# Kernel tuning notes

Measured on AMD Instinct MI355X. Metric: run time of the kernel, lower is better.

Reference implementation:

```python
import jax, jax.numpy as jnp
import numpy as np
import math

H = 8
KAPPA = 20.0
STAGES = 10
BN_EPS = 1e-5


def _l2norm(x, axis):
    return x / (1e-6 + jnp.linalg.norm(x, axis=axis, keepdims=True))


def _pmms(node, query_feature, mu0):
    # node: (b,c,n)  query_feature: (b,n,c)  mu0: (1,c,k)
    b = node.shape[0]
    mu = jnp.broadcast_to(mu0, (b, mu0.shape[1], mu0.shape[2]))

    def step(mu, _):
        z = jax.nn.softmax(KAPPA * jnp.einsum('bcn,bck->bnk', node, mu), axis=2)
        z = z / (1e-6 + z.sum(axis=1, keepdims=True))
        mu = _l2norm(jnp.einsum('bcn,bnk->bck', node, z), axis=1)
        return mu, None

    mu, _ = jax.lax.scan(step, mu, None, length=STAGES)
    mu = jax.lax.stop_gradient(mu)  # torch.no_grad in EM
    P = jax.lax.stop_gradient(
        jax.nn.softmax(jnp.einsum('bnc,bck->bnk', query_feature, mu), axis=2))
    return P, mu


def _conv2d_same(x, w):
    return jax.lax.conv_general_dilated(
        x, w, (1, 1), 'SAME', dimension_numbers=('NCHW', 'OIHW', 'NCHW'))


def _node_weight(x, cw1, cb1, g, be, cw2, cb2):
    # x: (b, n, ch) with n a perfect square
    b, n, ch = x.shape
    w = int(math.isqrt(n))
    y = x.transpose(0, 2, 1).reshape(b * ch, 1, w, w)
    y = _conv2d_same(y, cw1) + cb1[None, :, None, None]
    # eval-mode BatchNorm2d (running_mean=0, running_var=1)
    y = g[None, :, None, None] * (y / jnp.sqrt(1.0 + BN_EPS)) + be[None, :, None, None]
    y = jax.nn.relu(y)
    y = _conv2d_same(y, cw2) + cb2[None, :, None, None]
    y = jax.nn.sigmoid(y)
    y = y.reshape(b, ch, n).transpose(0, 2, 1)
    return x * y


def setup_inputs() -> dict:
    key = jax.random.key(0)
    ks = jax.random.split(key, 16)
    b, n, d = 16, 1024, 256
    s = 0.02
    mu_a = _l2norm(jax.random.normal(ks[6], (1, d, 5), jnp.float32) * math.sqrt(2.0 / 5), axis=1)
    mu_b = _l2norm(jax.random.normal(ks[7], (1, d, 2), jnp.float32) * math.sqrt(2.0 / 2), axis=1)
    return {
        'query': jax.random.normal(ks[0], (b, n, d), jnp.float32),
        'key': jax.random.normal(ks[1], (b, n, d), jnp.float32),
        'value': jax.random.normal(ks[2], (b, n), jnp.float32),
        'lamda': jax.random.uniform(ks[3], (1,), jnp.float32),
        'W0': jax.random.normal(ks[4], (d, d), jnp.float32) * s,
        'b0': jnp.zeros((d,), jnp.float32),
        'W1': jax.random.normal(ks[5], (d, d), jnp.float32) * s,
        'b1': jnp.zeros((d,), jnp.float32),
        'mu_a': mu_a,
        'mu_b': mu_b,
        'nw1_w1': jax.random.normal(ks[8], (16, 1, 3, 3), jnp.float32) * 0.1,
        'nw1_b1': jnp.zeros((16,), jnp.float32),
        'nw1_g': jnp.ones((16,), jnp.float32),
        'nw1_be': jnp.zeros((16,), jnp.float32),
        'nw1_w2': jax.random.normal(ks[9], (1, 16, 3, 3), jnp.float32) * 0.1,
        'nw1_b2': jnp.zeros((1,), jnp.float32),
        'nw2_w1': jax.random.normal(ks[10], (16, 1, 3, 3), jnp.float32) * 0.1,
        'nw2_b1': jnp.zeros((16,), jnp.float32),
        'nw2_g': jnp.ones((16,), jnp.float32),
        'nw2_be': jnp.zeros((16,), jnp.float32),
        'nw2_w2': jax.random.normal(ks[11], (1, 16, 3, 3), jnp.float32) * 0.1,
        'nw2_b2': jnp.zeros((1,), jnp.float32),
    }


def reference(query, key, value, lamda, W0, b0, W1, b1, mu_a, mu_b,
              nw1_w1, nw1_b1, nw1_g, nw1_be, nw1_w2, nw1_b2,
              nw2_w1, nw2_b1, nw2_g, nw2_be, nw2_w2, nw2_b2):
    b, n, d = query.shape
    dk = d // H
    scale = 1.0 / math.sqrt(dk)
    # linear projections, split heads: (b,H,n,dk)
    q_l = (query @ W0.T + b0).reshape(b, n, H, dk).transpose(0, 2, 1, 3)
    k_l = (key @ W1.T + b1).reshape(b, n, H, dk).transpose(0, 2, 1, 3)
    v = value[:, None, :, None]  # (b,1,n,1) broadcast over heads
    # global path: value-weighted mean key, elementwise multiply-reduce, relu
    key_global = jnp.mean(k_l * v, axis=-2, keepdims=True)  # (b,H,1,dk)
    whole = jax.nn.relu(jnp.sum(q_l * key_global, axis=-1, keepdims=True) * scale)
    whole = jnp.mean(whole, axis=-3)  # (b,n,1)
    # local path: standard softmax attention with scalar values (dropout eval=identity)
    scores = jnp.einsum('bhqd,bhkd->bhqk', q_l, k_l) * scale
    p_attn = jax.nn.softmax(scores, axis=-1)
    part = jnp.einsum('bhqk,bk->bhq', p_attn, value)[..., None]  # (b,H,n,1)
    part = jnp.mean(part, axis=-3)  # (b,n,1)
    f = (1.0 - lamda) * part + lamda * whole
    # PMMs prototype clustering
    qT = query.transpose(0, 2, 1)  # (b,c,n)
    P1, m1 = _pmms(qT, query, mu_a)   # (b,n,5), (b,c,5)
    P2, _ = _pmms(m1, query, mu_b)    # (b,n,2)
    q1 = _node_weight(P1, nw1_w1, nw1_b1, nw1_g, nw1_be, nw1_w2, nw1_b2)
    q2 = _node_weight(P2, nw2_w1, nw2_b1, nw2_g, nw2_be, nw2_w2, nw2_b2)
    # tree_drop eval=identity
    return jnp.concatenate((f, q1, q2), axis=-1)  # (b,n,8)
```

## Files before the change

### kernel.cpp

```cpp
#include <hip/hip_runtime.h>
#include <hip/hip_bf16.h>
#include <math.h>

#define NN 1024
#define ND 256
#define PSTRIDE 1288

typedef __hip_bfloat16 bf;
__device__ __forceinline__ float bf2f(bf h) { return __bfloat162float(h); }

typedef __attribute__((ext_vector_type(8))) short bf16x8;
typedef __attribute__((ext_vector_type(4))) float f32x4;

__device__ __forceinline__ float wave_reduce_sum(float v) {
#pragma unroll
    for (int off = 32; off > 0; off >>= 1) v += __shfl_down(v, off, 64);
    return v;
}
__device__ __forceinline__ float wave_allreduce_sum(float v) {
#pragma unroll
    for (int off = 1; off < 64; off <<= 1) v += __shfl_xor(v, off, 64);
    return v;
}

__global__ void zero_k(float* __restrict__ out) {
    int i = blockIdx.x * 1024 + threadIdx.x;
    out[(size_t)i * 8] = 0.f;
}

__global__ __launch_bounds__(256) void gemm2_k(
    const float* __restrict__ Aq, const float* __restrict__ Ak,
    const float* __restrict__ W0, const float* __restrict__ b0v,
    const float* __restrict__ W1, const float* __restrict__ b1v,
    bf* __restrict__ QL, bf* __restrict__ KL)
{
    const float* A; const float* Bw; const float* bias; bf* C;
    if (blockIdx.z == 0) { A = Aq; Bw = W0; bias = b0v; C = QL; }
    else                 { A = Ak; Bw = W1; bias = b1v; C = KL; }
    __shared__ short Ahi[4 * 64 * 8],  Alo[4 * 64 * 8];
    __shared__ short Bhi[16 * 64 * 8], Blo[16 * 64 * 8];
    const int t = threadIdx.x;
    const int wave = t >> 6, lane = t & 63;
    const int m0 = blockIdx.x * 64;

    f32x4 acc[4][4];
#pragma unroll
    for (int m = 0; m < 4; m++)
#pragma unroll
        for (int n = 0; n < 4; n++)
#pragma unroll
            for (int r = 0; r < 4; r++) acc[m][n][r] = 0.f;

    for (int k0 = 0; k0 < 256; k0 += 32) {
        __syncthreads();
        {
            int fm = t >> 6, ls = t & 63;
            const float* src = A + (size_t)(m0 + fm * 16 + (ls & 15)) * 256 + k0 + ((ls >> 4) * 8);
            float4 x = *(const float4*)src;
            float4 y = *(const float4*)(src + 4);
            float v[8] = {x.x, x.y, x.z, x.w, y.x, y.y, y.z, y.w};
            short h[8], l8[8];
#pragma unroll
            for (int j = 0; j < 8; j++) {
                bf hb = __float2bfloat16(v[j]);
                float hf = __bfloat162float(hb);
                bf lb = __float2bfloat16(v[j] - hf);
                h[j] = *(short*)&hb; l8[j] = *(short*)&lb;
            }
            *(bf16x8*)&Ahi[t * 8] = *(bf16x8*)h;
            *(bf16x8*)&Alo[t * 8] = *(bf16x8*)l8;
        }
#pragma unroll
        for (int i = 0; i < 4; i++) {
            int idx = t + i * 256;
            int nf = idx >> 6, ls = idx & 63;
            const float* src = Bw + (size_t)(nf * 16 + (ls & 15)) * 256 + k0 + ((ls >> 4) * 8);
            float4 x = *(const float4*)src;
            float4 y = *(const float4*)(src + 4);
            float v[8] = {x.x, x.y, x.z, x.w, y.x, y.y, y.z, y.w};
            short h[8], l8[8];
#pragma unroll
            for (int j = 0; j < 8; j++) {
                bf hb = __float2bfloat16(v[j]);
                float hf = __bfloat162float(hb);
                bf lb = __float2bfloat16(v[j] - hf);
                h[j] = *(short*)&hb; l8[j] = *(short*)&lb;
            }
            *(bf16x8*)&Bhi[idx * 8] = *(bf16x8*)h;
            *(bf16x8*)&Blo[idx * 8] = *(bf16x8*)l8;
        }
        __syncthreads();
        bf16x8 ah[4], al[4], bh[4], bl[4];
#pragma unroll
        for (int m = 0; m < 4; m++) {
            ah[m] = *(const bf16x8*)&Ahi[(m * 64 + lane) * 8];
            al[m] = *(const bf16x8*)&Alo[(m * 64 + lane) * 8];
        }
#pragma unroll
        for (int n = 0; n < 4; n++) {
            int nf = wave * 4 + n;
            bh[n] = *(const bf16x8*)&Bhi[(nf * 64 + lane) * 8];
            bl[n] = *(const bf16x8*)&Blo[(nf * 64 + lane) * 8];
        }
#pragma unroll
        for (int m = 0; m < 4; m++)
#pragma unroll
            for (int n = 0; n < 4; n++) {
                acc[m][n] = __builtin_amdgcn_mfma_f32_16x16x32_bf16(ah[m], bh[n], acc[m][n], 0, 0, 0);
                acc[m][n] = __builtin_amdgcn_mfma_f32_16x16x32_bf16(ah[m], bl[n], acc[m][n], 0, 0, 0);
                acc[m][n] = __builtin_amdgcn_mfma_f32_16x16x32_bf16(al[m], bh[n], acc[m][n], 0, 0, 0);
            }
    }
#pragma unroll
    for (int n = 0; n < 4; n++) {
        int col = (wave * 4 + n) * 16 + (lane & 15);
        float bv = bias[col];
#pragma unroll
        for (int m = 0; m < 4; m++) {
            int row = m0 + m * 16 + (lane >> 4) * 4;
#pragma unroll
            for (int r = 0; r < 4; r++) {
                bf hv = __float2bfloat16(acc[m][n][r] + bv);
                C[(size_t)(row + r) * 256 + col] = hv;
            }
        }
    }
}

__global__ __launch_bounds__(256) void attn3_k(
    const bf* __restrict__ QL, const bf* __restrict__ KL,
    const float* __restrict__ value, const float* __restrict__ lamda,
    float* __restrict__ out)
{
    const int bh = blockIdx.x; const int b = bh >> 3, h = bh & 7;
    const int t = threadIdx.x;
    const int wave = t >> 6, lane = t & 63;
    const int q0 = blockIdx.y * 256 + wave * 64;
    const float scale = 0.17677669529663687f;

    __shared__ bf Kf[128 * 32];
    __shared__ float vv[128];

    bf16x8 qf[4];
    {
        const bf* qbase = QL + ((size_t)b * NN) * ND + h * 32 + (lane >> 4) * 8;
#pragma unroll
        for (int m = 0; m < 4; m++)
            qf[m] = *(const bf16x8*)(qbase + (size_t)(q0 + m * 16 + (lane & 15)) * ND);
    }
    f32x4 lsum[4], vacc[4], wacc[4];
#pragma unroll
    for (int m = 0; m < 4; m++)
#pragma unroll
        for (int r = 0; r < 4; r++) { lsum[m][r] = 0.f; vacc[m][r] = 0.f; wacc[m][r] = 0.f; }

    const bf* kbase = KL + ((size_t)b * NN) * ND + h * 32;
    for (int kt = 0; kt < 8; kt++) {
        const int k0 = kt * 128;
        __syncthreads();
#pragma unroll
        for (int i = 0; i < 2; i++) {
            int f = t + i * 256;
            int row = ((f >> 6) << 4) + (f & 15);
            int chunk = (f >> 4) & 3;
            *(bf16x8*)&Kf[f * 8] = *(const bf16x8*)(kbase + (size_t)(k0 + row) * ND + chunk * 8);
        }
        if (t < 128) vv[t] = value[(size_t)b * NN + k0 + t];
        __syncthreads();
#pragma unroll
        for (int s = 0; s < 8; s++) {
            bf16x8 bfr = *(const bf16x8*)&Kf[(s * 64 + lane) * 8];
            float vcol = vv[s * 16 + (lane & 15)];
#pragma unroll
            for (int m = 0; m < 4; m++) {
                f32x4 acc = {0.f, 0.f, 0.f, 0.f};
                acc = __builtin_amdgcn_mfma_f32_16x16x32_bf16(qf[m], bfr, acc, 0, 0, 0);
#pragma unroll
                for (int r = 0; r < 4; r++) {
                    float sraw = acc[r];
                    float p = __expf(sraw * scale);
                    lsum[m][r] += p;
                    vacc[m][r] += p * vcol;
                    wacc[m][r] += sraw * vcol;
                }
            }
        }
    }
    const float lam = lamda[0];
#pragma unroll
    for (int m = 0; m < 4; m++)
#pragma unroll
        for (int r = 0; r < 4; r++) {
            float ls = lsum[m][r], va = vacc[m][r], wa = wacc[m][r];
#pragma unroll
            for (int off = 1; off < 16; off <<= 1) {
                ls += __shfl_xor(ls, off, 64);
                va += __shfl_xor(va, off, 64);
                wa += __shfl_xor(wa, off, 64);
            }
            if ((lane & 15) == 0) {
                int q = q0 + m * 16 + (lane >> 4) * 4 + r;
                float part = va / ls;
                float whole = fmaxf(wa * scale * (1.0f / 1024.0f), 0.f);
                float f = ((1.f - lam) * part + lam * whole) * 0.125f;
                atomicAdd(&out[((size_t)b * NN + q) * 8], f);
            }
        }
}

__global__ __launch_bounds__(256) void pmms_a_k(
    const float* __restrict__ query, const float* __restrict__ mu0a,
    const float* __restrict__ pin, float* __restrict__ pout, int stage)
{
    __shared__ float qs[64 * 260];
    __shared__ float muT[5 * 256];
    __shared__ float z_s[64][8];
    __shared__ float red[32];
    int chunk = blockIdx.x, b = blockIdx.y;
    int t = threadIdx.x;
    int wave = t >> 6, lane = t & 63;

    {
        const float* qg = query + ((size_t)b * NN + chunk * 64) * ND;
        for (int i = t; i < 4096; i += 256) {
            int row = i >> 6, c4 = (i & 63) * 4;
            *(float4*)&qs[row * 260 + c4] = *(const float4*)&qg[(size_t)row * ND + c4];
        }
    }

    if (stage == 0) {
        for (int idx = t; idx < 1280; idx += 256)
            muT[idx] = mu0a[(idx & 255) * 5 + (idx >> 8)];
    } else {
        float mr[5] = {0,0,0,0,0};
        float cs[5] = {0,0,0,0,0};
        for (int ch = 0; ch < 16; ch++) {
            const float* pb = pin + ((size_t)(b * 16 + ch)) * PSTRIDE;
#pragma unroll
            for (int k = 0; k < 5; k++) mr[k] += pb[k * 256 + t];
#pragma unroll
            for (int k = 0; k < 5; k++) cs[k] += pb[1280 + k];
        }
#pragma unroll
        for (int k = 0; k < 5; k++) mr[k] *= 1.0f / (1e-6f + cs[k]);
#pragma unroll
        for (int k = 0; k < 5; k++) {
            float s = wave_reduce_sum(mr[k] * mr[k]);
            if (lane == 0) red[wave * 5 + k] = s;
        }
        __syncthreads();
        if (t < 5) red[20 + t] = 1.0f / (1e-6f + sqrtf(red[t] + red[5 + t] + red[10 + t] + red[15 + t]));
        __syncthreads();
#pragma unroll
        for (int k = 0; k < 5; k++) muT[k * 256 + t] = mr[k] * red[20 + k];
    }
    __syncthreads();

    int n_local = t >> 2, part = t & 3;
    const float* qrow = &qs[n_local * 260 + part * 64];
    float lg[5] = {0,0,0,0,0};
#pragma unroll
    for (int c4 = 0; c4 < 64; c4 += 4) {
        float4 qv = *(const float4*)&qrow[c4];
#pragma unroll
        for (int k = 0; k < 5; k++) {
            float4 mv = *(const float4*)&muT[k * 256 + part * 64 + c4];
            lg[k] += qv.x*mv.x + qv.y*mv.y + qv.z*mv.z + qv.w*mv.w;
        }
    }
#pragma unroll
    for (int k = 0; k < 5; k++) {
        lg[k] += __shfl_xor(lg[k], 1, 64);
        lg[k] += __shfl_xor(lg[k], 2, 64);
    }
    float mx = lg[0];
#pragma unroll
    for (int k = 1; k < 5; k++) mx = fmaxf(mx, lg[k]);
    float e[5], ssum = 0.f;
#pragma unroll
    for (int k = 0; k < 5; k++) { e[k] = expf(20.0f * (lg[k] - mx)); ssum += e[k]; }
    float is = 1.0f / ssum;
    if (part == 0) {
#pragma unroll
        for (int k = 0; k < 5; k++) z_s[n_local][k] = e[k] * is;
    }
    __syncthreads();

    float pa[5] = {0,0,0,0,0};
#pragma unroll 4
    for (int nl = 0; nl < 64; nl++) {
        float qv = qs[nl * 260 + t];
        float4 z4 = *(const float4*)&z_s[nl][0];
        float z4v = z_s[nl][4];
        pa[0] += qv * z4.x; pa[1] += qv * z4.y; pa[2] += qv * z4.z;
        pa[3] += qv * z4.w; pa[4] += qv * z4v;
    }
    float* pb = pout + ((size_t)(b * 16 + chunk)) * PSTRIDE;
#pragma unroll
    for (int k = 0; k < 5; k++) pb[k * 256 + t] = pa[k];
    if (t < 5) {
        float s = 0.f;
        for (int nl = 0; nl < 64; nl++) s += z_s[nl][t];
        pb[1280 + t] = s;
    }
}

__global__ __launch_bounds__(64) void pmms_b_k(
    const float* __restrict__ pin, const float* __restrict__ mu0b,
    float* __restrict__ m1_ws, float* __restrict__ mu2_ws)
{
    int b = blockIdx.x, lane = threadIdx.x;
    float nd[5][4];
    float cs[5] = {0,0,0,0,0};
#pragma unroll
    for (int n = 0; n < 5; n++)
#pragma unroll
        for (int j = 0; j < 4; j++) nd[n][j] = 0.f;
    for (int ch = 0; ch < 16; ch++) {
        const float* pb = pin + ((size_t)(b * 16 + ch)) * PSTRIDE;
#pragma unroll
        for (int n = 0; n < 5; n++)
#pragma unroll
            for (int j = 0; j < 4; j++) nd[n][j] += pb[n * 256 + lane + 64 * j];
#pragma unroll
        for (int n = 0; n < 5; n++) cs[n] += pb[1280 + n];
    }
#pragma unroll
    for (int n = 0; n < 5; n++) {
        float inv = 1.0f / (1e-6f + cs[n]);
        float sq = 0.f;
#pragma unroll
        for (int j = 0; j < 4; j++) { nd[n][j] *= inv; sq += nd[n][j] * nd[n][j]; }
        float s = wave_allreduce_sum(sq);
        float nr = 1.0f / (1e-6f + sqrtf(s));
#pragma unroll
        for (int j = 0; j < 4; j++) {
            nd[n][j] *= nr;
            m1_ws[((size_t)b * 5 + n) * 256 + lane + 64 * j] = nd[n][j];
        }
    }
    float mu[2][4];
#pragma unroll
    for (int k = 0; k < 2; k++)
#pragma unroll
        for (int j = 0; j < 4; j++) mu[k][j] = mu0b[(lane + 64 * j) * 2 + k];
    for (int stage = 0; stage < 10; stage++) {
        float z[5][2];
        float colsum0 = 0.f, colsum1 = 0.f;
#pragma unroll
        for (int n = 0; n < 5; n++) {
            float l0 = 0.f, l1 = 0.f;
#pragma unroll
            for (int j = 0; j < 4; j++) { l0 += nd[n][j] * mu[0][j]; l1 += nd[n][j] * mu[1][j]; }
            l0 = wave_allreduce_sum(l0);
            l1 = wave_allreduce_sum(l1);
            float a0 = 20.0f * l0, a1 = 20.0f * l1;
            float mxv = fmaxf(a0, a1);
            float e0 = expf(a0 - mxv), e1 = expf(a1 - mxv);
            float inv = 1.0f / (e0 + e1);
            z[n][0] = e0 * inv; z[n][1] = e1 * inv;
            colsum0 += z[n][0]; colsum1 += z[n][1];
        }
        float i0 = 1.0f / (1e-6f + colsum0), i1 = 1.0f / (1e-6f + colsum1);
#pragma unroll
        for (int k = 0; k < 2; k++) {
            float iv = k ? i1 : i0;
            float sq = 0.f;
            float nm[4];
#pragma unroll
            for (int j = 0; j < 4; j++) {
                float v = 0.f;
#pragma unroll
                for (int n = 0; n < 5; n++) v += nd[n][j] * z[n][k];
                v *= iv;
                nm[j] = v; sq += v * v;
            }
            float s = wave_allreduce_sum(sq);
            float nr = 1.0f / (1e-6f + sqrtf(s));
#pragma unroll
            for (int j = 0; j < 4; j++) mu[k][j] = nm[j] * nr;
        }
    }
#pragma unroll
    for (int k = 0; k < 2; k++)
#pragma unroll
        for (int j = 0; j < 4; j++) mu2_ws[((size_t)b * 2 + k) * 256 + lane + 64 * j] = mu[k][j];
}

__global__ __launch_bounds__(256) void pmap_k(
    const float* __restrict__ query, const float* __restrict__ m1_ws,
    const float* __restrict__ mu2_ws, float* __restrict__ P1, float* __restrict__ P2)
{
    __shared__ float ms[7 * 256];
    int b = blockIdx.y;
    int t = threadIdx.x;
    int n = blockIdx.x * 256 + t;
    for (int idx = t; idx < 1280; idx += 256) ms[idx] = m1_ws[(size_t)b * 1280 + idx];
    for (int idx = t; idx < 512; idx += 256) ms[1280 + idx] = mu2_ws[(size_t)b * 512 + idx];
    __syncthreads();
    const float* qrow = query + ((size_t)b * NN + n) * ND;
    float lg[7] = {0,0,0,0,0,0,0};
    for (int c4 = 0; c4 < 256; c4 += 4) {
        float4 qv = *(const float4*)&qrow[c4];
#pragma unroll
        for (int k = 0; k < 7; k++) {
            float4 mv = *(const float4*)&ms[k * 256 + c4];
            lg[k] += qv.x*mv.x + qv.y*mv.y + qv.z*mv.z + qv.w*mv.w;
        }
    }
    float mx = lg[0];
#pragma unroll
    for (int k = 1; k < 5; k++) mx = fmaxf(mx, lg[k]);
    float e[5], ssum = 0.f;
#pragma unroll
    for (int k = 0; k < 5; k++) { e[k] = expf(lg[k] - mx); ssum += e[k]; }
    float is = 1.0f / ssum;
#pragma unroll
    for (int k = 0; k < 5; k++) P1[((size_t)b * 5 + k) * NN + n] = e[k] * is;
    float mx2 = fmaxf(lg[5], lg[6]);
    float e0 = expf(lg[5] - mx2), e1 = expf(lg[6] - mx2);
    float inv = 1.0f / (e0 + e1);
    P2[((size_t)b * 2 + 0) * NN + n] = e0 * inv;
    P2[((size_t)b * 2 + 1) * NN + n] = e1 * inv;
}

__global__ __launch_bounds__(1024) void nwconv_k(
    const float* __restrict__ P1, const float* __restrict__ P2,
    const float* __restrict__ w1a, const float* __restrict__ b1a,
    const float* __restrict__ ga,  const float* __restrict__ bea,
    const float* __restrict__ w2a, const float* __restrict__ b2a,
    const float* __restrict__ w1b, const float* __restrict__ b1b,
    const float* __restrict__ gb,  const float* __restrict__ beb,
    const float* __restrict__ w2b, const float* __restrict__ b2b,
    float* __restrict__ out)
{
    __shared__ float img[34 * 34];
    __shared__ float mid[16][34 * 34];
    __shared__ float w1s[144], w2s[144], bs[16], gs[16], bes[16], b2s[1];
    int ch = blockIdx.x, b = blockIdx.y;
    int t = threadIdx.x;
    int i = t >> 5, j = t & 31;
    const float* xsrc = (ch < 5) ? &P1[((size_t)b * 5 + ch) * NN]
                                 : &P2[((size_t)b * 2 + (ch - 5)) * NN];
    if (t < 144) { w1s[t] = (ch < 5 ? w1a : w1b)[t]; w2s[t] = (ch < 5 ? w2a : w2b)[t]; }
    if (t >= 256 && t < 272) {
        int y = t - 256;
        bs[y] = (ch < 5 ? b1a : b1b)[y];
        gs[y] = (ch < 5 ? ga : gb)[y];
        bes[y] = (ch < 5 ? bea : beb)[y];
    }
    if (t == 512) b2s[0] = (ch < 5 ? b2a : b2b)[0];
    for (int idx = t; idx < 1156; idx += 1024) img[idx] = 0.f;
    for (int idx = t; idx < 16 * 1156; idx += 1024) ((float*)mid)[idx] = 0.f;
    __syncthreads();
    float xv = xsrc[t];
    img[(i + 1) * 34 + (j + 1)] = xv;
    __syncthreads();
    float r[9];
#pragma unroll
    for (int dy = 0; dy < 3; dy++)
#pragma unroll
        for (int dx = 0; dx < 3; dx++)
            r[dy * 3 + dx] = img[(i + dy) * 34 + (j + dx)];
    const float bninv = rsqrtf(1.0f + 1e-5f);
#pragma unroll
    for (int oc = 0; oc < 16; oc++) {
        float a = 0.f;
#pragma unroll
        for (int q2 = 0; q2 < 9; q2++) a += w1s[oc * 9 + q2] * r[q2];
        a += bs[oc];
        a = gs[oc] * (a * bninv) + bes[oc];
        a = fmaxf(a, 0.f);
        mid[oc][(i + 1) * 34 + (j + 1)] = a;
    }
    __syncthreads();
    float acc2 = b2s[0];
#pragma unroll
    for (int oc = 0; oc < 16; oc++)
#pragma unroll
        for (int dy = 0; dy < 3; dy++)
#pragma unroll
            for (int dx = 0; dx < 3; dx++)
                acc2 += w2s[oc * 9 + dy * 3 + dx] * mid[oc][(i + dy) * 34 + (j + dx)];
    float sig = 1.0f / (1.0f + expf(-acc2));
    out[((size_t)(b * NN + t)) * 8 + 1 + ch] = xv * sig;
}

extern "C" void kernel_launch(void* const* d_in, const int* in_sizes, int n_in,
                              void* d_out, int out_size, void* d_ws, size_t ws_size,
                              hipStream_t stream) {
    const float* query = (const float*)d_in[0];
    const float* key   = (const float*)d_in[1];
    const float* value = (const float*)d_in[2];
    const float* lamda = (const float*)d_in[3];
    const float* W0 = (const float*)d_in[4];
    const float* b0 = (const float*)d_in[5];
    const float* W1 = (const float*)d_in[6];
    const float* b1 = (const float*)d_in[7];
    const float* mu_a = (const float*)d_in[8];
    const float* mu_b = (const float*)d_in[9];
    const float* nw1_w1 = (const float*)d_in[10];
    const float* nw1_b1 = (const float*)d_in[11];
    const float* nw1_g  = (const float*)d_in[12];
    const float* nw1_be = (const float*)d_in[13];
    const float* nw1_w2 = (const float*)d_in[14];
    const float* nw1_b2 = (const float*)d_in[15];
    const float* nw2_w1 = (const float*)d_in[16];
    const float* nw2_b1 = (const float*)d_in[17];
    const float* nw2_g  = (const float*)d_in[18];
    const float* nw2_be = (const float*)d_in[19];
    const float* nw2_w2 = (const float*)d_in[20];
    const float* nw2_b2 = (const float*)d_in[21];
    float* out = (float*)d_out;

    bf* QLb = (bf*)d_ws;
    bf* KLb = (bf*)((char*)d_ws + ((size_t)8 << 20));
    float* PA   = (float*)d_ws;
    float* PB   = PA + (size_t)16 * 16 * PSTRIDE;
    float* m1w  = PB + (size_t)16 * 16 * PSTRIDE;
    float* mu2w = m1w + (size_t)16 * 1280;
    float* P1w  = mu2w + (size_t)16 * 512;
    float* P2w  = P1w + (size_t)16 * 5 * 1024;

    zero_k<<<16, 1024, 0, stream>>>(out);
    gemm2_k<<<dim3(256, 1, 2), 256, 0, stream>>>(query, key, W0, b0, W1, b1, QLb, KLb);
    attn3_k<<<dim3(128, 4), 256, 0, stream>>>(QLb, KLb, value, lamda, out);
    for (int s = 0; s < 10; s++) {
        const float* pin = (s & 1) ? PA : PB;
        float* pout      = (s & 1) ? PB : PA;
        pmms_a_k<<<dim3(16, 16), 256, 0, stream>>>(query, mu_a, pin, pout, s);
    }
    pmms_b_k<<<16, 64, 0, stream>>>(PB, mu_b, m1w, mu2w);
    pmap_k<<<dim3(4, 16), 256, 0, stream>>>(query, m1w, mu2w, P1w, P2w);
    nwconv_k<<<dim3(7, 16), 1024, 0, stream>>>(P1w, P2w,
                                    nw1_w1, nw1_b1, nw1_g, nw1_be, nw1_w2, nw1_b2,
                                    nw2_w1, nw2_b1, nw2_g, nw2_be, nw2_w2, nw2_b2, out);
}
```

Baseline: 397.1 us.

## Fuse PMMs stages into one cooperative kernel and fold attention scale into QL

Replaces the ten per-stage PMMs launches, the second-level EM kernel and the probability-map kernel with a single cooperative kernel that keeps the query tile in LDS and uses grid-wide syncs between stages. This removes repeated launch overhead and the query reload on every stage. Separately, the attention scale times log2(e) is folded into the QL projection so attention can use exp2 directly, and the attention grid is doubled with half the rows per wave for more parallelism. Risks include grid-sync cost, co-residency requirements for the cooperative launch, and slight precision changes from bf16-rounding the scaled Q.

```diff
diff --git a/kernel.cpp b/kernel.cpp
--- a/kernel.cpp
+++ b/kernel.cpp
@@ -1,16 +1,21 @@
 #include <hip/hip_runtime.h>
 #include <hip/hip_bf16.h>
+#include <hip/hip_cooperative_groups.h>
 #include <math.h>
+
+namespace cg = cooperative_groups;
 
 #define NN 1024
 #define ND 256
 #define PSTRIDE 1288
 
 typedef __hip_bfloat16 bf;
-__device__ __forceinline__ float bf2f(bf h) { return __bfloat162float(h); }
 
 typedef __attribute__((ext_vector_type(8))) short bf16x8;
 typedef __attribute__((ext_vector_type(4))) float f32x4;
+
+#define QL_ALPHA 0.25503486216f
+#define WHOLE_LN2 0.6931471805599453f
 
 __device__ __forceinline__ float wave_reduce_sum(float v) {
 #pragma unroll
@@ -34,9 +39,9 @@
     const float* __restrict__ W1, const float* __restrict__ b1v,
     bf* __restrict__ QL, bf* __restrict__ KL)
 {
-    const float* A; const float* Bw; const float* bias; bf* C;
-    if (blockIdx.z == 0) { A = Aq; Bw = W0; bias = b0v; C = QL; }
-    else                 { A = Ak; Bw = W1; bias = b1v; C = KL; }
+    const float* A; const float* Bw; const float* bias; bf* C; float alpha;
+    if (blockIdx.z == 0) { A = Aq; Bw = W0; bias = b0v; C = QL; alpha = QL_ALPHA; }
+    else                 { A = Ak; Bw = W1; bias = b1v; C = KL; alpha = 1.0f; }
     __shared__ short Ahi[4 * 64 * 8],  Alo[4 * 64 * 8];
     __shared__ short Bhi[16 * 64 * 8], Blo[16 * 64 * 8];
     const int t = threadIdx.x;
@@ -120,14 +125,14 @@
             int row = m0 + m * 16 + (lane >> 4) * 4;
 #pragma unroll
             for (int r = 0; r < 4; r++) {
-                bf hv = __float2bfloat16(acc[m][n][r] + bv);
+                bf hv = __float2bfloat16((acc[m][n][r] + bv) * alpha);
                 C[(size_t)(row + r) * 256 + col] = hv;
             }
         }
     }
 }
 
-__global__ __launch_bounds__(256) void attn3_k(
+__global__ __launch_bounds__(256) void attn4_k(
     const bf* __restrict__ QL, const bf* __restrict__ KL,
     const float* __restrict__ value, const float* __restrict__ lamda,
     float* __restrict__ out)
@@ -135,22 +140,21 @@
     const int bh = blockIdx.x; const int b = bh >> 3, h = bh & 7;
     const int t = threadIdx.x;
     const int wave = t >> 6, lane = t & 63;
-    const int q0 = blockIdx.y * 256 + wave * 64;
-    const float scale = 0.17677669529663687f;
+    const int q0 = blockIdx.y * 128 + wave * 32;
 
     __shared__ bf Kf[128 * 32];
     __shared__ float vv[128];
 
-    bf16x8 qf[4];
+    bf16x8 qf[2];
     {
         const bf* qbase = QL + ((size_t)b * NN) * ND + h * 32 + (lane >> 4) * 8;
 #pragma unroll
-        for (int m = 0; m < 4; m++)
+        for (int m = 0; m < 2; m++)
             qf[m] = *(const bf16x8*)(qbase + (size_t)(q0 + m * 16 + (lane & 15)) * ND);
     }
-    f32x4 lsum[4], vacc[4], wacc[4];
-#pragma unroll
-    for (int m = 0; m < 4; m++)
+    f32x4 lsum[2], vacc[2], wacc[2];
+#pragma unroll
+    for (int m = 0; m < 2; m++)
 #pragma unroll
         for (int r = 0; r < 4; r++) { lsum[m][r] = 0.f; vacc[m][r] = 0.f; wacc[m][r] = 0.f; }
 
@@ -172,13 +176,13 @@
             bf16x8 bfr = *(const bf16x8*)&Kf[(s * 64 + lane) * 8];
             float vcol = vv[s * 16 + (lane & 15)];
 #pragma unroll
-            for (int m = 0; m < 4; m++) {
+            for (int m = 0; m < 2; m++) {
                 f32x4 acc = {0.f, 0.f, 0.f, 0.f};
                 acc = __builtin_amdgcn_mfma_f32_16x16x32_bf16(qf[m], bfr, acc, 0, 0, 0);
 #pragma unroll
                 for (int r = 0; r < 4; r++) {
                     float sraw = acc[r];
-                    float p = __expf(sraw * scale);
+                    float p = exp2f(sraw);
                     lsum[m][r] += p;
                     vacc[m][r] += p * vcol;
                     wacc[m][r] += sraw * vcol;
@@ -188,7 +192,7 @@
     }
     const float lam = lamda[0];
 #pragma unroll
-    for (int m = 0; m < 4; m++)
+    for (int m = 0; m < 2; m++)
 #pragma unroll
         for (int r = 0; r < 4; r++) {
             float ls = lsum[m][r], va = vacc[m][r], wa = wacc[m][r];
@@ -201,24 +205,30 @@
             if ((lane & 15) == 0) {
                 int q = q0 + m * 16 + (lane >> 4) * 4 + r;
                 float part = va / ls;
-                float whole = fmaxf(wa * scale * (1.0f / 1024.0f), 0.f);
+                float whole = fmaxf(wa * (WHOLE_LN2 / 1024.0f), 0.f);
                 float f = ((1.f - lam) * part + lam * whole) * 0.125f;
                 atomicAdd(&out[((size_t)b * NN + q) * 8], f);
             }
         }
 }
 
-__global__ __launch_bounds__(256) void pmms_a_k(
+__global__ __launch_bounds__(256) void pmms_coop_k(
     const float* __restrict__ query, const float* __restrict__ mu0a,
-    const float* __restrict__ pin, float* __restrict__ pout, int stage)
+    const float* __restrict__ mu0b,
+    float* __restrict__ PA, float* __restrict__ PB,
+    float* __restrict__ m1w, float* __restrict__ mu2w,
+    float* __restrict__ P1, float* __restrict__ P2)
 {
+    cg::grid_group gg = cg::this_grid();
     __shared__ float qs[64 * 260];
     __shared__ float muT[5 * 256];
+    __shared__ float ms2[512];
     __shared__ float z_s[64][8];
     __shared__ float red[32];
-    int chunk = blockIdx.x, b = blockIdx.y;
-    int t = threadIdx.x;
-    int wave = t >> 6, lane = t & 63;
+    const int chunk = blockIdx.x, b = blockIdx.y;
+    const int t = threadIdx.x;
+    const int wave = t >> 6, lane = t & 63;
+    const int n_local = t >> 2, part = t & 3;
 
     {
         const float* qg = query + ((size_t)b * NN + chunk * 64) * ND;
@@ -228,200 +238,215 @@
         }
     }
 
-    if (stage == 0) {
-        for (int idx = t; idx < 1280; idx += 256)
-            muT[idx] = mu0a[(idx & 255) * 5 + (idx >> 8)];
-    } else {
-        float mr[5] = {0,0,0,0,0};
+    for (int stage = 0; stage < 10; stage++) {
+        const float* pin = (stage & 1) ? PA : PB;
+        float* pout      = (stage & 1) ? PB : PA;
+        if (stage == 0) {
+            for (int idx = t; idx < 1280; idx += 256)
+                muT[idx] = mu0a[(idx & 255) * 5 + (idx >> 8)];
+        } else {
+            float mr[5] = {0,0,0,0,0};
+            float cs[5] = {0,0,0,0,0};
+            for (int ch = 0; ch < 16; ch++) {
+                const float* pb = pin + ((size_t)(b * 16 + ch)) * PSTRIDE;
+#pragma unroll
+                for (int k = 0; k < 5; k++) mr[k] += pb[k * 256 + t];
+#pragma unroll
+                for (int k = 0; k < 5; k++) cs[k] += pb[1280 + k];
+            }
+#pragma unroll
+            for (int k = 0; k < 5; k++) mr[k] *= 1.0f / (1e-6f + cs[k]);
+#pragma unroll
+            for (int k = 0; k < 5; k++) {
+                float s = wave_reduce_sum(mr[k] * mr[k]);
+                if (lane == 0) red[wave * 5 + k] = s;
+            }
+            __syncthreads();
+            if (t < 5) red[20 + t] = 1.0f / (1e-6f + sqrtf(red[t] + red[5 + t] + red[10 + t] + red[15 + t]));
+            __syncthreads();
+#pragma unroll
+            for (int k = 0; k < 5; k++) muT[k * 256 + t] = mr[k] * red[20 + k];
+        }
+        __syncthreads();
+
+        {
+            const float* qrow = &qs[n_local * 260 + part * 64];
+            float lg[5] = {0,0,0,0,0};
+#pragma unroll
+            for (int c4 = 0; c4 < 64; c4 += 4) {
+                float4 qv = *(const float4*)&qrow[c4];
+#pragma unroll
+                for (int k = 0; k < 5; k++) {
+                    float4 mv = *(const float4*)&muT[k * 256 + part * 64 + c4];
+                    lg[k] += qv.x*mv.x + qv.y*mv.y + qv.z*mv.z + qv.w*mv.w;
+                }
+            }
+#pragma unroll
+            for (int k = 0; k < 5; k++) {
+                lg[k] += __shfl_xor(lg[k], 1, 64);
+                lg[k] += __shfl_xor(lg[k], 2, 64);
+            }
+            float mx = lg[0];
+#pragma unroll
+            for (int k = 1; k < 5; k++) mx = fmaxf(mx, lg[k]);
+            float e[5], ssum = 0.f;
+#pragma unroll
+            for (int k = 0; k < 5; k++) { e[k] = expf(20.0f * (lg[k] - mx)); ssum += e[k]; }
+            float is = 1.0f / ssum;
+            if (part == 0) {
+#pragma unroll
+                for (int k = 0; k < 5; k++) z_s[n_local][k] = e[k] * is;
+            }
+        }
+        __syncthreads();
+
+        {
+            float pa[5] = {0,0,0,0,0};
+#pragma unroll 4
+            for (int nl = 0; nl < 64; nl++) {
+                float qv = qs[nl * 260 + t];
+                float4 z4 = *(const float4*)&z_s[nl][0];
+                float z4v = z_s[nl][4];
+                pa[0] += qv * z4.x; pa[1] += qv * z4.y; pa[2] += qv * z4.z;
+                pa[3] += qv * z4.w; pa[4] += qv * z4v;
+            }
+            float* pb = pout + ((size_t)(b * 16 + chunk)) * PSTRIDE;
+#pragma unroll
+            for (int k = 0; k < 5; k++) pb[k * 256 + t] = pa[k];
+            if (t < 5) {
+                float s = 0.f;
+                for (int nl = 0; nl < 64; nl++) s += z_s[nl][t];
+                pb[1280 + t] = s;
+            }
+        }
+        __threadfence();
+        gg.sync();
+    }
+
+    if (chunk == 0 && t < 64) {
+        const int ln = t;
+        float nd[5][4];
         float cs[5] = {0,0,0,0,0};
+#pragma unroll
+        for (int n = 0; n < 5; n++)
+#pragma unroll
+            for (int j = 0; j < 4; j++) nd[n][j] = 0.f;
         for (int ch = 0; ch < 16; ch++) {
-            const float* pb = pin + ((size_t)(b * 16 + ch)) * PSTRIDE;
-#pragma unroll
-            for (int k = 0; k < 5; k++) mr[k] += pb[k * 256 + t];
-#pragma unroll
-            for (int k = 0; k < 5; k++) cs[k] += pb[1280 + k];
-        }
-#pragma unroll
-        for (int k = 0; k < 5; k++) mr[k] *= 1.0f / (1e-6f + cs[k]);
-#pragma unroll
-        for (int k = 0; k < 5; k++) {
-            float s = wave_reduce_sum(mr[k] * mr[k]);
-            if (lane == 0) red[wave * 5 + k] = s;
-        }
-        __syncthreads();
-        if (t < 5) red[20 + t] = 1.0f / (1e-6f + sqrtf(red[t] + red[5 + t] + red[10 + t] + red[15 + t]));
-        __syncthreads();
-#pragma unroll
-        for (int k = 0; k < 5; k++) muT[k * 256 + t] = mr[k] * red[20 + k];
-    }
-    __syncthreads();
-
-    int n_local = t >> 2, part = t & 3;
-    const float* qrow = &qs[n_local * 260 + part * 64];
-    float lg[5] = {0,0,0,0,0};
-#pragma unroll
-    for (int c4 = 0; c4 < 64; c4 += 4) {
-        float4 qv = *(const float4*)&qrow[c4];
-#pragma unroll
-        for (int k = 0; k < 5; k++) {
-            float4 mv = *(const float4*)&muT[k * 256 + part * 64 + c4];
-            lg[k] += qv.x*mv.x + qv.y*mv.y + qv.z*mv.z + qv.w*mv.w;
-        }
-    }
-#pragma unroll
-    for (int k = 0; k < 5; k++) {
-        lg[k] += __shfl_xor(lg[k], 1, 64);
-        lg[k] += __shfl_xor(lg[k], 2, 64);
-    }
-    float mx = lg[0];
-#pragma unroll
-    for (int k = 1; k < 5; k++) mx = fmaxf(mx, lg[k]);
-    float e[5], ssum = 0.f;
-#pragma unroll
-    for (int k = 0; k < 5; k++) { e[k] = expf(20.0f * (lg[k] - mx)); ssum += e[k]; }
-    float is = 1.0f / ssum;
-    if (part == 0) {
-#pragma unroll
-        for (int k = 0; k < 5; k++) z_s[n_local][k] = e[k] * is;
-    }
-    __syncthreads();
-
-    float pa[5] = {0,0,0,0,0};
-#pragma unroll 4
-    for (int nl = 0; nl < 64; nl++) {
-        float qv = qs[nl * 260 + t];
-        float4 z4 = *(const float4*)&z_s[nl][0];
-        float z4v = z_s[nl][4];
-        pa[0] += qv * z4.x; pa[1] += qv * z4.y; pa[2] += qv * z4.z;
-        pa[3] += qv * z4.w; pa[4] += qv * z4v;
-    }
-    float* pb = pout + ((size_t)(b * 16 + chunk)) * PSTRIDE;
-#pragma unroll
-    for (int k = 0; k < 5; k++) pb[k * 256 + t] = pa[k];
-    if (t < 5) {
-        float s = 0.f;
-        for (int nl = 0; nl < 64; nl++) s += z_s[nl][t];
-        pb[1280 + t] = s;
-    }
-}
-
-__global__ __launch_bounds__(64) void pmms_b_k(
-    const float* __restrict__ pin, const float* __restrict__ mu0b,
-    float* __restrict__ m1_ws, float* __restrict__ mu2_ws)
-{
-    int b = blockIdx.x, lane = threadIdx.x;
-    float nd[5][4];
-    float cs[5] = {0,0,0,0,0};
-#pragma unroll
-    for (int n = 0; n < 5; n++)
-#pragma unroll
-        for (int j = 0; j < 4; j++) nd[n][j] = 0.f;
-    for (int ch = 0; ch < 16; ch++) {
-        const float* pb = pin + ((size_t)(b * 16 + ch)) * PSTRIDE;
-#pragma unroll
-        for (int n = 0; n < 5; n++)
-#pragma unroll
-            for (int j = 0; j < 4; j++) nd[n][j] += pb[n * 256 + lane + 64 * j];
-#pragma unroll
-        for (int n = 0; n < 5; n++) cs[n] += pb[1280 + n];
-    }
-#pragma unroll
-    for (int n = 0; n < 5; n++) {
-        float inv = 1.0f / (1e-6f + cs[n]);
-        float sq = 0.f;
-#pragma unroll
-        for (int j = 0; j < 4; j++) { nd[n][j] *= inv; sq += nd[n][j] * nd[n][j]; }
-        float s = wave_allreduce_sum(sq);
-        float nr = 1.0f / (1e-6f + sqrtf(s));
-#pragma unroll
-        for (int j = 0; j < 4; j++) {
-            nd[n][j] *= nr;
-            m1_ws[((size_t)b * 5 + n) * 256 + lane + 64 * j] = nd[n][j];
-        }
-    }
-    float mu[2][4];
-#pragma unroll
-    for (int k = 0; k < 2; k++)
-#pragma unroll
-        for (int j = 0; j < 4; j++) mu[k][j] = mu0b[(lane + 64 * j) * 2 + k];
-    for (int stage = 0; stage < 10; stage++) {
-        float z[5][2];
-        float colsum0 = 0.f, colsum1 = 0.f;
+            const float* pb = PB + ((size_t)(b * 16 + ch)) * PSTRIDE;
+#pragma unroll
+            for (int n = 0; n < 5; n++)
+#pragma unroll
+                for (int j = 0; j < 4; j++) nd[n][j] += pb[n * 256 + ln + 64 * j];
+#pragma unroll
+            for (int n = 0; n < 5; n++) cs[n] += pb[1280 + n];
+        }
 #pragma unroll
         for (int n = 0; n < 5; n++) {
-            float l0 = 0.f, l1 = 0.f;
-#pragma unroll
-            for (int j = 0; j < 4; j++) { l0 += nd[n][j] * mu[0][j]; l1 += nd[n][j] * mu[1][j]; }
-            l0 = wave_allreduce_sum(l0);
-            l1 = wave_allreduce_sum(l1);
-            float a0 = 20.0f * l0, a1 = 20.0f * l1;
-            float mxv = fmaxf(a0, a1);
-            float e0 = expf(a0 - mxv), e1 = expf(a1 - mxv);
-            float inv = 1.0f / (e0 + e1);
-            z[n][0] = e0 * inv; z[n][1] = e1 * inv;
-            colsum0 += z[n][0]; colsum1 += z[n][1];
-        }
-        float i0 = 1.0f / (1e-6f + colsum0), i1 = 1.0f / (1e-6f + colsum1);
-#pragma unroll
-        for (int k = 0; k < 2; k++) {
-            float iv = k ? i1 : i0;
+            float inv = 1.0f / (1e-6f + cs[n]);
             float sq = 0.f;
-            float nm[4];
-#pragma unroll
-            for (int j = 0; j < 4; j++) {
-                float v = 0.f;
-#pragma unroll
-                for (int n = 0; n < 5; n++) v += nd[n][j] * z[n][k];
-                v *= iv;
-                nm[j] = v; sq += v * v;
-            }
+#pragma unroll
+            for (int j = 0; j < 4; j++) { nd[n][j] *= inv; sq += nd[n][j] * nd[n][j]; }
             float s = wave_allreduce_sum(sq);
             float nr = 1.0f / (1e-6f + sqrtf(s));
 #pragma unroll
-            for (int j = 0; j < 4; j++) mu[k][j] = nm[j] * nr;
-        }
-    }
-#pragma unroll
-    for (int k = 0; k < 2; k++)
-#pragma unroll
-        for (int j = 0; j < 4; j++) mu2_ws[((size_t)b * 2 + k) * 256 + lane + 64 * j] = mu[k][j];
-}
-
-__global__ __launch_bounds__(256) void pmap_k(
-    const float* __restrict__ query, const float* __restrict__ m1_ws,
-    const float* __restrict__ mu2_ws, float* __restrict__ P1, float* __restrict__ P2)
-{
-    __shared__ float ms[7 * 256];
-    int b = blockIdx.y;
-    int t = threadIdx.x;
-    int n = blockIdx.x * 256 + t;
-    for (int idx = t; idx < 1280; idx += 256) ms[idx] = m1_ws[(size_t)b * 1280 + idx];
-    for (int idx = t; idx < 512; idx += 256) ms[1280 + idx] = mu2_ws[(size_t)b * 512 + idx];
+            for (int j = 0; j < 4; j++) {
+                nd[n][j] *= nr;
+                m1w[((size_t)b * 5 + n) * 256 + ln + 64 * j] = nd[n][j];
+            }
+        }
+        float mu[2][4];
+#pragma unroll
+        for (int k = 0; k < 2; k++)
+#pragma unroll
+            for (int j = 0; j < 4; j++) mu[k][j] = mu0b[(ln + 64 * j) * 2 + k];
+        for (int stage = 0; stage < 10; stage++) {
+            float z[5][2];
+            float colsum0 = 0.f, colsum1 = 0.f;
+#pragma unroll
+            for (int n = 0; n < 5; n++) {
+                float l0 = 0.f, l1 = 0.f;
+#pragma unroll
+                for (int j = 0; j < 4; j++) { l0 += nd[n][j] * mu[0][j]; l1 += nd[n][j] * mu[1][j]; }
+                l0 = wave_allreduce_sum(l0);
+                l1 = wave_allreduce_sum(l1);
+                float a0 = 20.0f * l0, a1 = 20.0f * l1;
+                float mxv = fmaxf(a0, a1);
+                float e0 = expf(a0 - mxv), e1 = expf(a1 - mxv);
+                float inv = 1.0f / (e0 + e1);
+                z[n][0] = e0 * inv; z[n][1] = e1 * inv;
+                colsum0 += z[n][0]; colsum1 += z[n][1];
+            }
+            float i0 = 1.0f / (1e-6f + colsum0), i1 = 1.0f / (1e-6f + colsum1);
+#pragma unroll
+            for (int k = 0; k < 2; k++) {
+                float iv = k ? i1 : i0;
+                float sq = 0.f;
+                float nm[4];
+#pragma unroll
+                for (int j = 0; j < 4; j++) {
+                    float v = 0.f;
+#pragma unroll
+                    for (int n = 0; n < 5; n++) v += nd[n][j] * z[n][k];
+                    v *= iv;
+                    nm[j] = v; sq += v * v;
+                }
+                float s = wave_allreduce_sum(sq);
+                float nr = 1.0f / (1e-6f + sqrtf(s));
+#pragma unroll
+                for (int j = 0; j < 4; j++) mu[k][j] = nm[j] * nr;
+            }
+        }
+#pragma unroll
+        for (int k = 0; k < 2; k++)
+#pragma unroll
+            for (int j = 0; j < 4; j++) mu2w[((size_t)b * 2 + k) * 256 + ln + 64 * j] = mu[k][j];
+    }
+    __threadfence();
+    gg.sync();
+
+    for (int idx = t; idx < 1280; idx += 256) muT[idx] = m1w[(size_t)b * 1280 + idx];
+    for (int idx = t; idx < 512; idx += 256) ms2[idx] = mu2w[(size_t)b * 512 + idx];
     __syncthreads();
-    const float* qrow = query + ((size_t)b * NN + n) * ND;
-    float lg[7] = {0,0,0,0,0,0,0};
-    for (int c4 = 0; c4 < 256; c4 += 4) {
-        float4 qv = *(const float4*)&qrow[c4];
+    {
+        const float* qrow = &qs[n_local * 260 + part * 64];
+        float lg[7] = {0,0,0,0,0,0,0};
+#pragma unroll
+        for (int c4 = 0; c4 < 64; c4 += 4) {
+            float4 qv = *(const float4*)&qrow[c4];
+#pragma unroll
+            for (int k = 0; k < 5; k++) {
+                float4 mv = *(const float4*)&muT[k * 256 + part * 64 + c4];
+                lg[k] += qv.x*mv.x + qv.y*mv.y + qv.z*mv.z + qv.w*mv.w;
+            }
+#pragma unroll
+            for (int k = 0; k < 2; k++) {
+                float4 mv = *(const float4*)&ms2[k * 256 + part * 64 + c4];
+                lg[5 + k] += qv.x*mv.x + qv.y*mv.y + qv.z*mv.z + qv.w*mv.w;
+            }
+        }
 #pragma unroll
         for (int k = 0; k < 7; k++) {
-            float4 mv = *(const float4*)&ms[k * 256 + c4];
-            lg[k] += qv.x*mv.x + qv.y*mv.y + qv.z*mv.z + qv.w*mv.w;
-        }
-    }
-    float mx = lg[0];
-#pragma unroll
-    for (int k = 1; k < 5; k++) mx = fmaxf(mx, lg[k]);
-    float e[5], ssum = 0.f;
-#pragma unroll
-    for (int k = 0; k < 5; k++) { e[k] = expf(lg[k] - mx); ssum += e[k]; }
-    float is = 1.0f / ssum;
-#pragma unroll
-    for (int k = 0; k < 5; k++) P1[((size_t)b * 5 + k) * NN + n] = e[k] * is;
-    float mx2 = fmaxf(lg[5], lg[6]);
-    float e0 = expf(lg[5] - mx2), e1 = expf(lg[6] - mx2);
-    float inv = 1.0f / (e0 + e1);
-    P2[((size_t)b * 2 + 0) * NN + n] = e0 * inv;
-    P2[((size_t)b * 2 + 1) * NN + n] = e1 * inv;
+            lg[k] += __shfl_xor(lg[k], 1, 64);
+            lg[k] += __shfl_xor(lg[k], 2, 64);
+        }
+        if (part == 0) {
+            int n = chunk * 64 + n_local;
+            float mx = lg[0];
+#pragma unroll
+            for (int k = 1; k < 5; k++) mx = fmaxf(mx, lg[k]);
+            float e[5], ssum = 0.f;
+#pragma unroll
+            for (int k = 0; k < 5; k++) { e[k] = expf(lg[k] - mx); ssum += e[k]; }
+            float is = 1.0f / ssum;
+#pragma unroll
+            for (int k = 0; k < 5; k++) P1[((size_t)b * 5 + k) * NN + n] = e[k] * is;
+            float mx2 = fmaxf(lg[5], lg[6]);
+            float e0 = expf(lg[5] - mx2), e1 = expf(lg[6] - mx2);
+            float inv = 1.0f / (e0 + e1);
+            P2[((size_t)b * 2 + 0) * NN + n] = e0 * inv;
+            P2[((size_t)b * 2 + 1) * NN + n] = e1 * inv;
+        }
+    }
 }
 
 __global__ __launch_bounds__(1024) void nwconv_k(
@@ -524,14 +549,18 @@
 
     zero_k<<<16, 1024, 0, stream>>>(out);
     gemm2_k<<<dim3(256, 1, 2), 256, 0, stream>>>(query, key, W0, b0, W1, b1, QLb, KLb);
-    attn3_k<<<dim3(128, 4), 256, 0, stream>>>(QLb, KLb, value, lamda, out);
-    for (int s = 0; s < 10; s++) {
-        const float* pin = (s & 1) ? PA : PB;
-        float* pout      = (s & 1) ? PB : PA;
-        pmms_a_k<<<dim3(16, 16), 256, 0, stream>>>(query, mu_a, pin, pout, s);
-    }
-    pmms_b_k<<<16, 64, 0, stream>>>(PB, mu_b, m1w, mu2w);
-    pmap_k<<<dim3(4, 16), 256, 0, stream>>>(query, m1w, mu2w, P1w, P2w);
+    attn4_k<<<dim3(128, 8), 256, 0, stream>>>(QLb, KLb, value, lamda, out);
+
+    {
+        void* args[] = {
+            (void*)&query, (void*)&mu_a, (void*)&mu_b,
+            (void*)&PA, (void*)&PB, (void*)&m1w, (void*)&mu2w,
+            (void*)&P1w, (void*)&P2w
+        };
+        hipLaunchCooperativeKernel((void*)pmms_coop_k, dim3(16, 16), dim3(256),
+                                   args, 0, stream);
+    }
+
     nwconv_k<<<dim3(7, 16), 1024, 0, stream>>>(P1w, P2w,
                                     nw1_w1, nw1_b1, nw1_g, nw1_be, nw1_w2, nw1_b2,
                                     nw2_w1, nw2_b1, nw2_g, nw2_be, nw2_w2, nw2_b2, out);
```

Result: slower. 1.003 ms (+152.5%).
